# Optimization experiments

Measured on AMD Instinct MI355X. Metric: run time of the kernel, lower is better.

The kernel has to match this reference:

```python
import jax, jax.numpy as jnp
import numpy as np

B = 32768
H = 512
NH = 8
EPS = 1e-5


def _glorot(key, shape):
    fan_in, fan_out = shape[-1], shape[0]
    lim = (6.0 / (fan_in + fan_out)) ** 0.5
    return jax.random.uniform(key, shape, jnp.float32, -lim, lim)


def setup_inputs() -> dict:
    key = jax.random.key(0)
    ks = jax.random.split(key, 32)
    d = {
        "graph_features": jax.random.normal(ks[0], (B, H), jnp.float32),
        "seq_features": jax.random.normal(ks[1], (B, H), jnp.float32),
        "tabular_features": jax.random.normal(ks[2], (B, H), jnp.float32),
    }
    i = 3
    for name in ("g2s", "s2g", "t2m"):
        d[f"{name}_w_in"] = _glorot(ks[i], (3 * H, H)); i += 1
        d[f"{name}_b_in"] = jnp.zeros((3 * H,), jnp.float32)
        d[f"{name}_w_out"] = _glorot(ks[i], (H, H)); i += 1
        d[f"{name}_b_out"] = jnp.zeros((H,), jnp.float32)
    for name in ("gate_g", "gate_s", "gate_t"):
        d[f"{name}_w"] = _glorot(ks[i], (H, 2 * H)); i += 1
        d[f"{name}_b"] = jnp.zeros((H,), jnp.float32)
    d["fc1_w"] = _glorot(ks[i], (2 * H, 3 * H)); i += 1
    d["fc1_b"] = jnp.zeros((2 * H,), jnp.float32)
    d["ln_g"] = jnp.ones((2 * H,), jnp.float32)
    d["ln_b"] = jnp.zeros((2 * H,), jnp.float32)
    d["fc2_w"] = _glorot(ks[i], (H, 2 * H)); i += 1
    d["fc2_b"] = jnp.zeros((H,), jnp.float32)
    return d


def _mha(q, k, v, w_in, b_in, w_out, b_out):
    # q: [B,Sq,H], k/v: [B,Sk,H]. PyTorch nn.MultiheadAttention math (eval mode).
    dh = H // NH
    qp = q @ w_in[:H].T + b_in[:H]
    kp = k @ w_in[H:2 * H].T + b_in[H:2 * H]
    vp = v @ w_in[2 * H:].T + b_in[2 * H:]
    qh = qp.reshape(qp.shape[0], qp.shape[1], NH, dh)
    kh = kp.reshape(kp.shape[0], kp.shape[1], NH, dh)
    vh = vp.reshape(vp.shape[0], vp.shape[1], NH, dh)
    scores = jnp.einsum("bqhd,bkhd->bhqk", qh, kh) / jnp.sqrt(jnp.float32(dh))
    attn = jax.nn.softmax(scores, axis=-1)
    out = jnp.einsum("bhqk,bkhd->bqhd", attn, vh).reshape(q.shape[0], q.shape[1], H)
    return out @ w_out.T + b_out


def reference(graph_features, seq_features, tabular_features,
              g2s_w_in, g2s_b_in, g2s_w_out, g2s_b_out,
              s2g_w_in, s2g_b_in, s2g_w_out, s2g_b_out,
              t2m_w_in, t2m_b_in, t2m_w_out, t2m_b_out,
              gate_g_w, gate_g_b, gate_s_w, gate_s_b, gate_t_w, gate_t_b,
              fc1_w, fc1_b, ln_g, ln_b, fc2_w, fc2_b):
    g = graph_features[:, None, :]   # [B,1,H]
    s = seq_features[:, None, :]
    t = tabular_features[:, None, :]

    graph_to_seq = _mha(s, g, g, g2s_w_in, g2s_b_in, g2s_w_out, g2s_b_out)
    seq_to_graph = _mha(g, s, s, s2g_w_in, s2g_b_in, s2g_w_out, s2g_b_out)

    graph_gate = jax.nn.sigmoid(jnp.concatenate([g, seq_to_graph], -1) @ gate_g_w.T + gate_g_b)
    seq_gate = jax.nn.sigmoid(jnp.concatenate([s, graph_to_seq], -1) @ gate_s_w.T + gate_s_b)
    gated_graph = g * graph_gate
    gated_seq = s * seq_gate

    multimodal = jnp.concatenate([gated_graph, gated_seq], axis=1)  # [B,2,H]
    t2m = _mha(multimodal, t, t, t2m_w_in, t2m_b_in, t2m_w_out, t2m_b_out)  # [B,2,H]

    tab_comb = jnp.concatenate([t, t2m.mean(axis=1, keepdims=True)], -1)
    tab_gate = jax.nn.sigmoid(tab_comb @ gate_t_w.T + gate_t_b)
    gated_tab = t * tab_gate

    allf = jnp.concatenate([gated_graph[:, 0], gated_seq[:, 0], gated_tab[:, 0]], -1)  # [B,3H]
    h = allf @ fc1_w.T + fc1_b
    mu = h.mean(-1, keepdims=True)
    var = ((h - mu) ** 2).mean(-1, keepdims=True)
    h = (h - mu) / jnp.sqrt(var + EPS) * ln_g + ln_b
    h = jax.nn.relu(h)
    return h @ fc2_w.T + fc2_b
```

## Files before the change

### kernel.cpp

```cpp
#include <hip/hip_runtime.h>
#include <stdint.h>
#include <stddef.h>

#define MROWS 32768
#define HDIM  512
#define BM 128
#define BN 128
#define BK 64

typedef __attribute__((ext_vector_type(8))) _Float16 half8;
typedef __attribute__((ext_vector_type(4))) _Float16 half4v;
typedef __attribute__((ext_vector_type(4))) float    f32x4;

static __device__ __forceinline__ void gld_lds16(const void* g, void* l) {
    __builtin_amdgcn_global_load_lds(
        (__attribute__((address_space(1))) void*)(uintptr_t)g,
        (__attribute__((address_space(3))) void*)(uint32_t)(uintptr_t)l,
        16, 0, 0);
}

struct CvtJob  { const float* src; _Float16* dst; int srcld4, dstld, rowlen4, rows; };
struct CvtJobs { CvtJob j[11]; };

__global__ __launch_bounds__(256)
void cvt_rows(CvtJobs J) {
    const CvtJob jb = J.j[blockIdx.y];
    const int row = blockIdx.x;
    if (row >= jb.rows) return;
    const float4* __restrict__ s = (const float4*)jb.src + (size_t)row * jb.srcld4;
    _Float16* __restrict__ d = jb.dst + (size_t)row * jb.dstld;
    for (int c = threadIdx.x; c < jb.rowlen4; c += 256) {
        const float4 v = s[c];
        half4v o = { (_Float16)v.x, (_Float16)v.y, (_Float16)v.z, (_Float16)v.w };
        *(half4v*)(d + c * 4) = o;
    }
}

__global__ __launch_bounds__(384)
void cvt_chunk3(const float* __restrict__ x0, const float* __restrict__ x1,
                const float* __restrict__ x2, _Float16* __restrict__ dst) {
    const int row = blockIdx.x;
    const int mod = threadIdx.x >> 7;
    const int c   = threadIdx.x & 127;
    const float* s = (mod == 0) ? x0 : (mod == 1) ? x1 : x2;
    const float4 v = ((const float4*)(s + (size_t)row * 512))[c];
    half4v o = { (_Float16)v.x, (_Float16)v.y, (_Float16)v.z, (_Float16)v.w };
    *(half4v*)(dst + (size_t)row * 1536 + mod * 512 + c * 4) = o;
}

struct TcvtArgs { const float* src[3]; _Float16* dst; };
__global__ __launch_bounds__(256)
void tcvt512(TcvtArgs a) {
    __shared__ float t[32][33];
    const int m = blockIdx.z;
    const float* __restrict__ src = a.src[m];
    _Float16* __restrict__ dst = a.dst + (size_t)m * HDIM * HDIM;
    const int bx = blockIdx.x * 32, by = blockIdx.y * 32;
    const int tx = threadIdx.x & 31, ty = threadIdx.x >> 5;
    #pragma unroll
    for (int q = 0; q < 4; ++q)
        t[ty + q * 8][tx] = src[(size_t)(by + ty + q * 8) * 512 + bx + tx];
    __syncthreads();
    #pragma unroll
    for (int q = 0; q < 4; ++q)
        dst[(size_t)(bx + ty + q * 8) * 512 + by + tx] = (_Float16)t[tx][ty + q * 8];
}

struct MvArgs { const float* W[3]; const float* x[3]; const float* b[3]; float* y; int ldw, woff; };
__global__ __launch_bounds__(256)
void mv3(MvArgs a) {
    const int m = blockIdx.y;
    const int i = blockIdx.x * 256 + threadIdx.x;
    const float* __restrict__ W = a.W[m] + (size_t)i * a.ldw + a.woff;
    const float* __restrict__ x = a.x[m];
    float s = a.b[m][i];
    for (int j = 0; j < 512; ++j) s += W[j] * x[j];
    a.y[m * 512 + i] = s;
}

struct GemmP {
    const void* A1;
    const _Float16* W; const float* bias; void* C;
    int K, ldA1, ldw, ldc, coff;
    int zsA, zsW, zsC;
};

template<int EPI, int OCC>
__global__ __launch_bounds__(256, OCC)
void gemm_k(GemmP p) {
    __shared__ __align__(16) unsigned char smem[32768];
    _Float16* Asm = (_Float16*)smem;
    _Float16* Bsm = (_Float16*)(smem + 16384);

    const int tid  = threadIdx.x;
    const int wid  = tid >> 6;
    const int lane = tid & 63;
    const int m0 = blockIdx.x * BM;
    const int n0 = blockIdx.y * BN;
    const ptrdiff_t zz = blockIdx.z;
    const _Float16* __restrict__ A1h = (const _Float16*)((const char*)p.A1 + zz * p.zsA);
    const _Float16* __restrict__ Wp  = (const _Float16*)((const char*)p.W + zz * p.zsW);
    char* Cz = (char*)p.C + zz * p.zsC;

    const int wr = (wid >> 1) * 64;
    const int wc = (wid & 1) * 64;
    const int l15 = lane & 15;
    const int lhi = lane >> 4;

    f32x4 acc[4][4] = {};
    half8 xsave[8];
    const int colsel = (tid & 15) * 8;
    const int xtile  = n0 + (colsel & 64);
    const int xco    = colsel & 63;

    for (int kt = 0; kt < p.K; kt += BK) {
        #pragma unroll
        for (int i = 0; i < 4; ++i) {
            const int seg = wid * 256 + i * 64 + lane;
            const int row = seg >> 3;
            const int ke  = (seg & 7) * 8;
            gld_lds16(Wp  + (size_t)(n0 + row) * p.ldw  + kt + ke, &Bsm[seg * 8]);
            gld_lds16(A1h + (size_t)(m0 + row) * p.ldA1 + kt + ke, &Asm[seg * 8]);
        }
        __syncthreads();
        if (EPI == 1 && kt == xtile) {
            #pragma unroll
            for (int q = 0; q < 8; ++q)
                xsave[q] = *(const half8*)&Asm[(q * 16 + (tid >> 4)) * BK + xco];
        }
        #pragma unroll
        for (int kk = 0; kk < BK; kk += 32) {
            half8 fa[4], fb[4];
            #pragma unroll
            for (int i = 0; i < 4; ++i) {
                fa[i] = *(const half8*)&Asm[(wr + i * 16 + l15) * BK + kk + lhi * 8];
                fb[i] = *(const half8*)&Bsm[(wc + i * 16 + l15) * BK + kk + lhi * 8];
            }
            #pragma unroll
            for (int i = 0; i < 4; ++i)
                #pragma unroll
                for (int j = 0; j < 4; ++j)
                    acc[i][j] = __builtin_amdgcn_mfma_f32_16x16x32_f16(fa[i], fb[j], acc[i][j], 0, 0, 0);
        }
        __syncthreads();
    }

    if (EPI == 3) {
        float* Cf = (float*)smem;
        float* __restrict__ C = (float*)Cz;
        #pragma unroll
        for (int h = 0; h < 2; ++h) {
            if ((wr >> 6) == h) {
                #pragma unroll
                for (int j = 0; j < 4; ++j) {
                    const int col = wc + j * 16 + l15;
                    const float bia = p.bias ? p.bias[n0 + col] : 0.f;
                    #pragma unroll
                    for (int i = 0; i < 4; ++i)
                        #pragma unroll
                        for (int r = 0; r < 4; ++r)
                            Cf[(i * 16 + lhi * 4 + r) * 128 + col] = acc[i][j][r] + bia;
                }
            }
            __syncthreads();
            #pragma unroll
            for (int pph = 0; pph < 8; ++pph) {
                const int seg = pph * 256 + tid;
                const int row = seg >> 5, cs = seg & 31;
                const float4 v = *(const float4*)&Cf[row * 128 + cs * 4];
                *(float4*)&C[(size_t)(m0 + h * 64 + row) * p.ldc + n0 + cs * 4] = v;
            }
            __syncthreads();
        }
    } else {
        _Float16* Ct = (_Float16*)smem;
        #pragma unroll
        for (int j = 0; j < 4; ++j) {
            const int col = wc + j * 16 + l15;
            const float bia = (EPI == 2) ? 0.f : (p.bias ? p.bias[n0 + col] : 0.f);
            #pragma unroll
            for (int i = 0; i < 4; ++i)
                #pragma unroll
                for (int r = 0; r < 4; ++r) {
                    float v = acc[i][j][r] + bia;
                    if (EPI == 1) v = 1.f / (1.f + __expf(-v));
                    Ct[(wr + i * 16 + lhi * 4 + r) * 128 + col] = (_Float16)v;
                }
        }
        __syncthreads();
        _Float16* __restrict__ C = (_Float16*)Cz;
        #pragma unroll
        for (int pph = 0; pph < 8; ++pph) {
            const int seg = pph * 256 + tid;
            const int row = seg >> 4, cs = seg & 15;
            half8 hv = *(const half8*)&Ct[row * 128 + cs * 8];
            const size_t cidx = (size_t)(m0 + row) * p.ldc + p.coff + n0 + cs * 8;
            if (EPI == 1) hv = hv * xsave[pph];
            if (EPI == 2) { const half8 old = *(const half8*)&C[cidx]; hv = hv + old; }
            *(half8*)&C[cidx] = hv;
        }
    }
}

__global__ __launch_bounds__(256)
void ln_relu(_Float16* __restrict__ h, const float* __restrict__ gamma,
             const float* __restrict__ beta) {
    const int row  = blockIdx.x * 4 + (threadIdx.x >> 6);
    const int lane = threadIdx.x & 63;
    _Float16* hr = h + (size_t)row * 1024;
    const half8 v0 = *(const half8*)(hr + lane * 8);
    const half8 v1 = *(const half8*)(hr + 512 + lane * 8);
    float f0[8], f1[8];
    float s = 0.f, s2 = 0.f;
    #pragma unroll
    for (int j = 0; j < 8; ++j) {
        f0[j] = (float)v0[j]; s += f0[j]; s2 += f0[j] * f0[j];
        f1[j] = (float)v1[j]; s += f1[j]; s2 += f1[j] * f1[j];
    }
    #pragma unroll
    for (int off = 32; off > 0; off >>= 1) {
        s  += __shfl_xor(s,  off, 64);
        s2 += __shfl_xor(s2, off, 64);
    }
    const float mean = s * (1.f / 1024.f);
    const float var  = s2 * (1.f / 1024.f) - mean * mean;
    const float rstd = rsqrtf(var + 1e-5f);
    half8 o0, o1;
    #pragma unroll
    for (int j = 0; j < 8; ++j) {
        const int i0 = lane * 8 + j, i1 = 512 + lane * 8 + j;
        const float av = (f0[j] - mean) * rstd * gamma[i0] + beta[i0];
        const float bv = (f1[j] - mean) * rstd * gamma[i1] + beta[i1];
        o0[j] = (_Float16)(av > 0.f ? av : 0.f);
        o1[j] = (_Float16)(bv > 0.f ? bv : 0.f);
    }
    *(half8*)(hr + lane * 8) = o0;
    *(half8*)(hr + 512 + lane * 8) = o1;
}

__global__ __launch_bounds__(256)
void copy_f32(const float4* __restrict__ src, float4* __restrict__ dst, int n4) {
    const int stride = gridDim.x * blockDim.x;
    for (int i = blockIdx.x * blockDim.x + threadIdx.x; i < n4; i += stride)
        dst[i] = src[i];
}

extern "C" void kernel_launch(void* const* d_in, const int* in_sizes, int n_in,
                              void* d_out, int out_size, void* d_ws, size_t ws_size,
                              hipStream_t stream)
{
    (void)in_sizes; (void)n_in; (void)out_size;
    const size_t HH = (size_t)HDIM * HDIM;
    const size_t WBYTES = 25 * HH * 2 + 2 * 3 * 512 * 4;

    int CH = 16384;
    if (ws_size < 2 * (size_t)CH * 1536 * 2 + WBYTES) CH = 8192;
    if (ws_size < 2 * (size_t)CH * 1536 * 2 + WBYTES) return;
    const int nch = MROWS / CH;

    _Float16* wsH   = (_Float16*)d_ws;
    _Float16* slotB = wsH;
    _Float16* Xch   = slotB + (size_t)CH * 1536;
    _Float16* Wouth = Xch   + (size_t)CH * 1536;
    _Float16* Wg2h  = Wouth + 3 * HH;
    _Float16* WvT   = Wg2h  + 3 * HH;
    _Float16* WcoT  = WvT   + 3 * HH;
    _Float16* Wbig  = WcoT  + 3 * HH;
    _Float16* Wc2   = Wbig  + 4 * HH;
    _Float16* fc1h  = Wc2   + 1 * HH;
    _Float16* fc2h  = fc1h  + 6 * HH;
    float*    bco   = (float*)(fc2h + 2 * HH);
    float*    beff  = bco + 3 * 512;

    const float* X[3] = { (const float*)d_in[0], (const float*)d_in[1], (const float*)d_in[2] };
    const int asrc[3] = { 1, 0, 2 };

    CvtJobs cj;
    for (int m = 0; m < 3; ++m) {
        cj.j[m]     = { (const float*)d_in[5 + 4 * m], Wouth + m * HH, 128, 512, 128, 512 };
        cj.j[3 + m] = { (const float*)d_in[15 + 2 * m] + 512, Wg2h + m * HH, 256, 512, 128, 512 };
    }
    cj.j[6]  = { (const float*)d_in[15], Wbig,                    256, 1024, 128, 512 };
    cj.j[7]  = { (const float*)d_in[17], Wbig + 512 * 1024 + 512, 256, 1024, 128, 512 };
    cj.j[8]  = { (const float*)d_in[19], Wc2,                     256, 512,  128, 512 };
    cj.j[9]  = { (const float*)d_in[21], fc1h, 384, 1536, 384, 1024 };
    cj.j[10] = { (const float*)d_in[25], fc2h, 256, 1024, 256, 512 };
    cvt_rows<<<dim3(1024, 11, 1), 256, 0, stream>>>(cj);

    TcvtArgs ta;
    for (int m = 0; m < 3; ++m) ta.src[m] = (const float*)d_in[3 + 4 * m] + 2 * HH;
    ta.dst = WvT;
    tcvt512<<<dim3(16, 16, 3), 256, 0, stream>>>(ta);

    MvArgs mv;
    for (int m = 0; m < 3; ++m) {
        mv.W[m] = (const float*)d_in[5 + 4 * m];
        mv.x[m] = (const float*)d_in[4 + 4 * m] + 2 * HDIM;
        mv.b[m] = (const float*)d_in[6 + 4 * m];
    }
    mv.y = bco; mv.ldw = 512; mv.woff = 0;
    mv3<<<dim3(2, 3, 1), 256, 0, stream>>>(mv);

    GemmP p;
    p.bias = nullptr; p.coff = 0;
    p.zsA = p.zsW = p.zsC = 0;

    p.A1 = WvT; p.ldA1 = 512;
    p.W = Wouth; p.ldw = 512;
    p.C = WcoT; p.ldc = 512;
    p.K = 512;
    p.zsA = (int)(HH * 2); p.zsW = (int)(HH * 2); p.zsC = (int)(HH * 2);
    gemm_k<0, 4><<<dim3(4, 4, 3), 256, 0, stream>>>(p);

    p.A1 = Wg2h; p.zsA = (int)(HH * 2);
    p.W = WcoT + HH; p.zsW = -(int)(HH * 2);
    p.C = Wbig + 512; p.ldc = 1024; p.zsC = (int)((512 * 1024 - 512) * 2);
    gemm_k<0, 4><<<dim3(4, 4, 2), 256, 0, stream>>>(p);

    p.A1 = Wg2h + 2 * HH; p.zsA = 0;
    p.W = WcoT + 2 * HH; p.zsW = 0;
    p.C = Wc2; p.ldc = 512; p.zsC = 0;
    gemm_k<2, 4><<<dim3(4, 4, 1), 256, 0, stream>>>(p);

    for (int m = 0; m < 3; ++m) {
        mv.W[m] = (const float*)d_in[15 + 2 * m];
        mv.x[m] = bco + asrc[m] * 512;
        mv.b[m] = (const float*)d_in[16 + 2 * m];
    }
    mv.y = beff; mv.ldw = 1024; mv.woff = 512;
    mv3<<<dim3(2, 3, 1), 256, 0, stream>>>(mv);

    _Float16* hbuf = (_Float16*)d_out;
    for (int c = 0; c < nch; ++c) {
        const size_t roff = (size_t)c * CH;

        cvt_chunk3<<<dim3(CH, 1, 1), 384, 0, stream>>>(
            X[0] + roff * HDIM, X[1] + roff * HDIM, X[2] + roff * HDIM, Xch);

        p.A1 = Xch; p.ldA1 = 1536;
        p.W = Wbig; p.ldw = 1024;
        p.bias = beff;
        p.C = slotB; p.ldc = 1536; p.coff = 0;
        p.K = 1024;
        gemm_k<1, 3><<<dim3(CH / BM, 1024 / BN, 1), 256, 0, stream>>>(p);

        p.A1 = Xch + 1024; p.ldA1 = 1536;
        p.W = Wc2; p.ldw = 512;
        p.bias = beff + 1024;
        p.C = slotB; p.ldc = 1536; p.coff = 1024;
        p.K = 512;
        gemm_k<1, 3><<<dim3(CH / BM, HDIM / BN, 1), 256, 0, stream>>>(p);

        p.A1 = slotB; p.ldA1 = 1536;
        p.W = fc1h; p.ldw = 1536;
        p.bias = (const float*)d_in[22];
        p.C = hbuf + roff * 1024; p.ldc = 1024; p.coff = 0;
        p.K = 1536;
        gemm_k<0, 4><<<dim3(CH / BM, 1024 / BN, 1), 256, 0, stream>>>(p);
    }

    ln_relu<<<dim3(MROWS / 4, 1, 1), 256, 0, stream>>>(
        hbuf, (const float*)d_in[23], (const float*)d_in[24]);

    for (int c = 0; c < 2; ++c) {
        const size_t roff = (size_t)c * 16384;
        p.A1 = hbuf + roff * 1024; p.ldA1 = 1024;
        p.W = fc2h; p.ldw = 1024;
        p.bias = (const float*)d_in[26];
        p.C = d_ws; p.ldc = HDIM; p.coff = 0;
        p.K = 1024;
        gemm_k<3, 4><<<dim3(16384 / BM, HDIM / BN, 1), 256, 0, stream>>>(p);

        copy_f32<<<dim3(1024, 1, 1), 256, 0, stream>>>(
            (const float4*)d_ws, (float4*)d_out + roff * HDIM / 4,
            (int)((size_t)16384 * HDIM / 4));
    }
}
```

Baseline: 520.6 us.

## Merge gate GEMMs into one launch and write fc2 output directly

```diff
diff --git a/kernel.cpp b/kernel.cpp
--- a/kernel.cpp
+++ b/kernel.cpp
@@ -4,6 +4,7 @@
 
 #define MROWS 32768
 #define HDIM  512
+#define CH    16384
 #define BM 128
 #define BN 128
 #define BK 64
@@ -83,9 +84,11 @@
     const _Float16* W; const float* bias; void* C;
     int K, ldA1, ldw, ldc, coff;
     int zsA, zsW, zsC;
+    const void* A1b; const _Float16* Wb; const float* biasb;
+    int Kb, ldwb, coffb, nyb;
 };
 
-template<int EPI, int OCC>
+template<int EPI, int OCC, int MERGED>
 __global__ __launch_bounds__(256, OCC)
 void gemm_k(GemmP p) {
     __shared__ __align__(16) unsigned char smem[32768];
@@ -97,10 +100,24 @@
     const int lane = tid & 63;
     const int m0 = blockIdx.x * BM;
     const int n0 = blockIdx.y * BN;
-    const ptrdiff_t zz = blockIdx.z;
-    const _Float16* __restrict__ A1h = (const _Float16*)((const char*)p.A1 + zz * p.zsA);
-    const _Float16* __restrict__ Wp  = (const _Float16*)((const char*)p.W + zz * p.zsW);
-    char* Cz = (char*)p.C + zz * p.zsC;
+
+    const _Float16* __restrict__ A1h;
+    const _Float16* __restrict__ Wp;
+    const float* biasp;
+    char* Cz;
+    int K, ldA1, ldw, coff;
+    if (MERGED && blockIdx.z == 1) {
+        if ((int)blockIdx.y >= p.nyb) return;
+        A1h = (const _Float16*)p.A1b; Wp = p.Wb; biasp = p.biasb;
+        Cz = (char*)p.C; K = p.Kb; ldA1 = p.ldA1; ldw = p.ldwb; coff = p.coffb;
+    } else {
+        const ptrdiff_t zz = MERGED ? 0 : (ptrdiff_t)blockIdx.z;
+        A1h = (const _Float16*)((const char*)p.A1 + zz * p.zsA);
+        Wp  = (const _Float16*)((const char*)p.W + zz * p.zsW);
+        biasp = p.bias;
+        Cz = (char*)p.C + zz * p.zsC;
+        K = p.K; ldA1 = p.ldA1; ldw = p.ldw; coff = p.coff;
+    }
 
     const int wr = (wid >> 1) * 64;
     const int wc = (wid & 1) * 64;
@@ -113,14 +130,14 @@
     const int xtile  = n0 + (colsel & 64);
     const int xco    = colsel & 63;
 
-    for (int kt = 0; kt < p.K; kt += BK) {
+    for (int kt = 0; kt < K; kt += BK) {
         #pragma unroll
         for (int i = 0; i < 4; ++i) {
             const int seg = wid * 256 + i * 64 + lane;
             const int row = seg >> 3;
             const int ke  = (seg & 7) * 8;
-            gld_lds16(Wp  + (size_t)(n0 + row) * p.ldw  + kt + ke, &Bsm[seg * 8]);
-            gld_lds16(A1h + (size_t)(m0 + row) * p.ldA1 + kt + ke, &Asm[seg * 8]);
+            gld_lds16(Wp  + (size_t)(n0 + row) * ldw  + kt + ke, &Bsm[seg * 8]);
+            gld_lds16(A1h + (size_t)(m0 + row) * ldA1 + kt + ke, &Asm[seg * 8]);
         }
         __syncthreads();
         if (EPI == 1 && kt == xtile) {
@@ -154,7 +171,7 @@
                 #pragma unroll
                 for (int j = 0; j < 4; ++j) {
                     const int col = wc + j * 16 + l15;
-                    const float bia = p.bias ? p.bias[n0 + col] : 0.f;
+                    const float bia = biasp ? biasp[n0 + col] : 0.f;
                     #pragma unroll
                     for (int i = 0; i < 4; ++i)
                         #pragma unroll
@@ -177,7 +194,7 @@
         #pragma unroll
         for (int j = 0; j < 4; ++j) {
             const int col = wc + j * 16 + l15;
-            const float bia = (EPI == 2) ? 0.f : (p.bias ? p.bias[n0 + col] : 0.f);
+            const float bia = (EPI == 2) ? 0.f : (biasp ? biasp[n0 + col] : 0.f);
             #pragma unroll
             for (int i = 0; i < 4; ++i)
                 #pragma unroll
@@ -194,7 +211,7 @@
             const int seg = pph * 256 + tid;
             const int row = seg >> 4, cs = seg & 15;
             half8 hv = *(const half8*)&Ct[row * 128 + cs * 8];
-            const size_t cidx = (size_t)(m0 + row) * p.ldc + p.coff + n0 + cs * 8;
+            const size_t cidx = (size_t)(m0 + row) * p.ldc + coff + n0 + cs * 8;
             if (EPI == 1) hv = hv * xsave[pph];
             if (EPI == 2) { const half8 old = *(const half8*)&C[cidx]; hv = hv + old; }
             *(half8*)&C[cidx] = hv;
@@ -203,11 +220,12 @@
 }
 
 __global__ __launch_bounds__(256)
-void ln_relu(_Float16* __restrict__ h, const float* __restrict__ gamma,
-             const float* __restrict__ beta) {
+void ln_relu(const _Float16* __restrict__ hin, _Float16* __restrict__ hout,
+             const float* __restrict__ gamma, const float* __restrict__ beta) {
     const int row  = blockIdx.x * 4 + (threadIdx.x >> 6);
     const int lane = threadIdx.x & 63;
-    _Float16* hr = h + (size_t)row * 1024;
+    const _Float16* hr = hin + (size_t)row * 1024;
+    _Float16* ho = hout + (size_t)row * 1024;
     const half8 v0 = *(const half8*)(hr + lane * 8);
     const half8 v1 = *(const half8*)(hr + 512 + lane * 8);
     float f0[8], f1[8];
@@ -234,15 +252,8 @@
         o0[j] = (_Float16)(av > 0.f ? av : 0.f);
         o1[j] = (_Float16)(bv > 0.f ? bv : 0.f);
     }
-    *(half8*)(hr + lane * 8) = o0;
-    *(half8*)(hr + 512 + lane * 8) = o1;
-}
-
-__global__ __launch_bounds__(256)
-void copy_f32(const float4* __restrict__ src, float4* __restrict__ dst, int n4) {
-    const int stride = gridDim.x * blockDim.x;
-    for (int i = blockIdx.x * blockDim.x + threadIdx.x; i < n4; i += stride)
-        dst[i] = src[i];
+    *(half8*)(ho + lane * 8) = o0;
+    *(half8*)(ho + 512 + lane * 8) = o1;
 }
 
 extern "C" void kernel_launch(void* const* d_in, const int* in_sizes, int n_in,
@@ -251,12 +262,6 @@
 {
     (void)in_sizes; (void)n_in; (void)out_size;
     const size_t HH = (size_t)HDIM * HDIM;
-    const size_t WBYTES = 25 * HH * 2 + 2 * 3 * 512 * 4;
-
-    int CH = 16384;
-    if (ws_size < 2 * (size_t)CH * 1536 * 2 + WBYTES) CH = 8192;
-    if (ws_size < 2 * (size_t)CH * 1536 * 2 + WBYTES) return;
-    const int nch = MROWS / CH;
 
     _Float16* wsH   = (_Float16*)d_ws;
     _Float16* slotB = wsH;
@@ -271,6 +276,9 @@
     _Float16* fc2h  = fc1h  + 6 * HH;
     float*    bco   = (float*)(fc2h + 2 * HH);
     float*    beff  = bco + 3 * 512;
+    _Float16* hws   = wsH;
+    const size_t need = (size_t)((char*)(beff + 3 * 512) - (char*)d_ws);
+    if (ws_size < need) return;
 
     const float* X[3] = { (const float*)d_in[0], (const float*)d_in[1], (const float*)d_in[2] };
     const int asrc[3] = { 1, 0, 2 };
@@ -304,23 +312,25 @@
     GemmP p;
     p.bias = nullptr; p.coff = 0;
     p.zsA = p.zsW = p.zsC = 0;
+    p.A1b = nullptr; p.Wb = nullptr; p.biasb = nullptr;
+    p.Kb = 0; p.ldwb = 0; p.coffb = 0; p.nyb = 0;
 
     p.A1 = WvT; p.ldA1 = 512;
     p.W = Wouth; p.ldw = 512;
     p.C = WcoT; p.ldc = 512;
     p.K = 512;
     p.zsA = (int)(HH * 2); p.zsW = (int)(HH * 2); p.zsC = (int)(HH * 2);
-    gemm_k<0, 4><<<dim3(4, 4, 3), 256, 0, stream>>>(p);
+    gemm_k<0, 4, 0><<<dim3(4, 4, 3), 256, 0, stream>>>(p);
 
     p.A1 = Wg2h; p.zsA = (int)(HH * 2);
     p.W = WcoT + HH; p.zsW = -(int)(HH * 2);
     p.C = Wbig + 512; p.ldc = 1024; p.zsC = (int)((512 * 1024 - 512) * 2);
-    gemm_k<0, 4><<<dim3(4, 4, 2), 256, 0, stream>>>(p);
+    gemm_k<0, 4, 0><<<dim3(4, 4, 2), 256, 0, stream>>>(p);
 
     p.A1 = Wg2h + 2 * HH; p.zsA = 0;
     p.W = WcoT + 2 * HH; p.zsW = 0;
     p.C = Wc2; p.ldc = 512; p.zsC = 0;
-    gemm_k<2, 4><<<dim3(4, 4, 1), 256, 0, stream>>>(p);
+    gemm_k<2, 4, 0><<<dim3(4, 4, 1), 256, 0, stream>>>(p);
 
     for (int m = 0; m < 3; ++m) {
         mv.W[m] = (const float*)d_in[15 + 2 * m];
@@ -331,7 +341,7 @@
     mv3<<<dim3(2, 3, 1), 256, 0, stream>>>(mv);
 
     _Float16* hbuf = (_Float16*)d_out;
-    for (int c = 0; c < nch; ++c) {
+    for (int c = 0; c < 2; ++c) {
         const size_t roff = (size_t)c * CH;
 
         cvt_chunk3<<<dim3(CH, 1, 1), 384, 0, stream>>>(
@@ -342,37 +352,25 @@
         p.bias = beff;
         p.C = slotB; p.ldc = 1536; p.coff = 0;
         p.K = 1024;
-        gemm_k<1, 3><<<dim3(CH / BM, 1024 / BN, 1), 256, 0, stream>>>(p);
-
-        p.A1 = Xch + 1024; p.ldA1 = 1536;
-        p.W = Wc2; p.ldw = 512;
-        p.bias = beff + 1024;
-        p.C = slotB; p.ldc = 1536; p.coff = 1024;
-        p.K = 512;
-        gemm_k<1, 3><<<dim3(CH / BM, HDIM / BN, 1), 256, 0, stream>>>(p);
+        p.A1b = Xch + 1024; p.Wb = Wc2; p.biasb = beff + 1024;
+        p.Kb = 512; p.ldwb = 512; p.coffb = 1024; p.nyb = 4;
+        gemm_k<1, 3, 1><<<dim3(CH / BM, 1024 / BN, 2), 256, 0, stream>>>(p);
 
         p.A1 = slotB; p.ldA1 = 1536;
         p.W = fc1h; p.ldw = 1536;
         p.bias = (const float*)d_in[22];
         p.C = hbuf + roff * 1024; p.ldc = 1024; p.coff = 0;
         p.K = 1536;
-        gemm_k<0, 4><<<dim3(CH / BM, 1024 / BN, 1), 256, 0, stream>>>(p);
+        gemm_k<0, 4, 0><<<dim3(CH / BM, 1024 / BN, 1), 256, 0, stream>>>(p);
     }
 
     ln_relu<<<dim3(MROWS / 4, 1, 1), 256, 0, stream>>>(
-        hbuf, (const float*)d_in[23], (const float*)d_in[24]);
-
-    for (int c = 0; c < 2; ++c) {
-        const size_t roff = (size_t)c * 16384;
-        p.A1 = hbuf + roff * 1024; p.ldA1 = 1024;
-        p.W = fc2h; p.ldw = 1024;
-        p.bias = (const float*)d_in[26];
-        p.C = d_ws; p.ldc = HDIM; p.coff = 0;
-        p.K = 1024;
-        gemm_k<3, 4><<<dim3(16384 / BM, HDIM / BN, 1), 256, 0, stream>>>(p);
-
-        copy_f32<<<dim3(1024, 1, 1), 256, 0, stream>>>(
-            (const float4*)d_ws, (float4*)d_out + roff * HDIM / 4,
-            (int)((size_t)16384 * HDIM / 4));
-    }
-}
+        hbuf, hws, (const float*)d_in[23], (const float*)d_in[24]);
+
+    p.A1 = hws; p.ldA1 = 1024;
+    p.W = fc2h; p.ldw = 1024;
+    p.bias = (const float*)d_in[26];
+    p.C = d_out; p.ldc = HDIM; p.coff = 0;
+    p.K = 1024;
+    gemm_k<3, 4, 0><<<dim3(MROWS / BM, HDIM / BN, 1), 256, 0, stream>>>(p);
+}
```

Measured after the change: 454.1 us. 1.15x faster.

## Add 256x256 double-buffered swizzled GEMM and drop fc2 copy staging

Applied to the files above, without the earlier changes.

```diff
diff --git a/kernel.cpp b/kernel.cpp
--- a/kernel.cpp
+++ b/kernel.cpp
@@ -4,6 +4,7 @@
 
 #define MROWS 32768
 #define HDIM  512
+#define CH    16384
 #define BM 128
 #define BN 128
 #define BK 64
@@ -97,7 +98,7 @@
     const int lane = tid & 63;
     const int m0 = blockIdx.x * BM;
     const int n0 = blockIdx.y * BN;
-    const ptrdiff_t zz = blockIdx.z;
+    const ptrdiff_t zz = (ptrdiff_t)blockIdx.z;
     const _Float16* __restrict__ A1h = (const _Float16*)((const char*)p.A1 + zz * p.zsA);
     const _Float16* __restrict__ Wp  = (const _Float16*)((const char*)p.W + zz * p.zsW);
     char* Cz = (char*)p.C + zz * p.zsC;
@@ -108,10 +109,6 @@
     const int lhi = lane >> 4;
 
     f32x4 acc[4][4] = {};
-    half8 xsave[8];
-    const int colsel = (tid & 15) * 8;
-    const int xtile  = n0 + (colsel & 64);
-    const int xco    = colsel & 63;
 
     for (int kt = 0; kt < p.K; kt += BK) {
         #pragma unroll
@@ -123,11 +120,6 @@
             gld_lds16(A1h + (size_t)(m0 + row) * p.ldA1 + kt + ke, &Asm[seg * 8]);
         }
         __syncthreads();
-        if (EPI == 1 && kt == xtile) {
-            #pragma unroll
-            for (int q = 0; q < 8; ++q)
-                xsave[q] = *(const half8*)&Asm[(q * 16 + (tid >> 4)) * BK + xco];
-        }
         #pragma unroll
         for (int kk = 0; kk < BK; kk += 32) {
             half8 fa[4], fb[4];
@@ -195,19 +187,152 @@
             const int row = seg >> 4, cs = seg & 15;
             half8 hv = *(const half8*)&Ct[row * 128 + cs * 8];
             const size_t cidx = (size_t)(m0 + row) * p.ldc + p.coff + n0 + cs * 8;
-            if (EPI == 1) hv = hv * xsave[pph];
+            if (EPI == 1) {
+                const half8 xv = *(const half8*)(A1h + (size_t)(m0 + row) * p.ldA1
+                                                 + n0 + cs * 8);
+                hv = hv * xv;
+            }
             if (EPI == 2) { const half8 old = *(const half8*)&C[cidx]; hv = hv + old; }
             *(half8*)&C[cidx] = hv;
         }
     }
 }
 
+struct Gemm8P {
+    const _Float16* A; const _Float16* W; const float* bias; _Float16* C;
+    int K, ldA, ldW, ldc, coff;
+};
+
+template<int EPI>
+__global__ __launch_bounds__(512, 1)
+void gemm8(Gemm8P p) {
+    __shared__ __align__(16) unsigned char lds[131072];
+    char* LA = (char*)lds;
+    char* LB = (char*)lds + 65536;
+
+    const int tid  = threadIdx.x;
+    const int wid  = tid >> 6;
+    const int lane = tid & 63;
+    const int wm = wid >> 2;
+    const int wn = wid & 3;
+    const int l15 = lane & 15;
+    const int lhi = lane >> 4;
+    const int m0 = blockIdx.x * 256;
+    const int n0 = blockIdx.y * 256;
+    const _Float16* __restrict__ A = p.A;
+    const _Float16* __restrict__ W = p.W;
+    const int ldA = p.ldA, ldW = p.ldW;
+    const int nT = p.K >> 6;
+
+    f32x4 acc[8][4] = {};
+
+    auto stage = [&](int t) {
+        const int q = t & 1;
+        const int kt = t * 64;
+        #pragma unroll
+        for (int k = 0; k < 4; ++k) {
+            const int u = tid + k * 512;
+            const int row = u >> 3;
+            const int sc = (u & 7) ^ (row & 7);
+            gld_lds16(A + (size_t)(m0 + row) * ldA + kt + sc * 8,
+                      LA + ((size_t)q * 2048 + u) * 16);
+        }
+        #pragma unroll
+        for (int k = 0; k < 4; ++k) {
+            const int u = tid + k * 512;
+            const int row = u >> 3;
+            const int sc = (u & 7) ^ (row & 7);
+            gld_lds16(W + (size_t)(n0 + row) * ldW + kt + sc * 8,
+                      LB + ((size_t)q * 2048 + u) * 16);
+        }
+    };
+
+    stage(0);
+    asm volatile("s_waitcnt vmcnt(0)" ::: "memory");
+    __builtin_amdgcn_s_barrier();
+    asm volatile("" ::: "memory");
+
+    for (int t = 0; t < nT; ++t) {
+        const size_t aq = (size_t)(t & 1) * 2048 * 16;
+        half8 fb[4][2];
+        #pragma unroll
+        for (int ph = 0; ph < 4; ++ph) {
+            half8 fa[2][2];
+            if (ph == 0) {
+                #pragma unroll
+                for (int nf = 0; nf < 4; ++nf)
+                    #pragma unroll
+                    for (int kh = 0; kh < 2; ++kh) {
+                        const int row = wn * 64 + nf * 16 + l15;
+                        const int c16 = (kh * 4 + lhi) ^ (row & 7);
+                        fb[nf][kh] = *(const half8*)(LB + aq + ((size_t)row * 8 + c16) * 16);
+                    }
+            }
+            #pragma unroll
+            for (int mi = 0; mi < 2; ++mi)
+                #pragma unroll
+                for (int kh = 0; kh < 2; ++kh) {
+                    const int row = wm * 128 + (ph * 2 + mi) * 16 + l15;
+                    const int c16 = (kh * 4 + lhi) ^ (row & 7);
+                    fa[mi][kh] = *(const half8*)(LA + aq + ((size_t)row * 8 + c16) * 16);
+                }
+            if (ph == 0 && t + 1 < nT) stage(t + 1);
+            asm volatile("" ::: "memory");
+            __builtin_amdgcn_s_barrier();
+            asm volatile("s_waitcnt lgkmcnt(0)" ::: "memory");
+            __builtin_amdgcn_sched_barrier(0);
+            __builtin_amdgcn_s_setprio(1);
+            #pragma unroll
+            for (int mi = 0; mi < 2; ++mi)
+                #pragma unroll
+                for (int nf = 0; nf < 4; ++nf)
+                    #pragma unroll
+                    for (int kh = 0; kh < 2; ++kh)
+                        acc[ph * 2 + mi][nf] = __builtin_amdgcn_mfma_f32_16x16x32_f16(
+                            fa[mi][kh], fb[nf][kh], acc[ph * 2 + mi][nf], 0, 0, 0);
+            __builtin_amdgcn_s_setprio(0);
+            if (ph == 3) asm volatile("s_waitcnt vmcnt(0)" ::: "memory");
+            asm volatile("" ::: "memory");
+            __builtin_amdgcn_s_barrier();
+            asm volatile("" ::: "memory");
+        }
+    }
+
+    _Float16* Ct = (_Float16*)lds;
+    #pragma unroll
+    for (int mf = 0; mf < 8; ++mf)
+        #pragma unroll
+        for (int nf = 0; nf < 4; ++nf) {
+            const int col = wn * 64 + nf * 16 + l15;
+            const float bia = p.bias[n0 + col];
+            #pragma unroll
+            for (int r = 0; r < 4; ++r) {
+                float v = acc[mf][nf][r] + bia;
+                if (EPI == 1) v = 1.f / (1.f + __expf(-v));
+                Ct[(wm * 128 + mf * 16 + lhi * 4 + r) * 256 + col] = (_Float16)v;
+            }
+        }
+    __syncthreads();
+    #pragma unroll
+    for (int it = 0; it < 16; ++it) {
+        const int u = it * 512 + tid;
+        const int row = u >> 5, cs = u & 31;
+        half8 hv = *(const half8*)&Ct[row * 256 + cs * 8];
+        if (EPI == 1) {
+            const half8 xv = *(const half8*)(A + (size_t)(m0 + row) * ldA + n0 + cs * 8);
+            hv = hv * xv;
+        }
+        *(half8*)&p.C[(size_t)(m0 + row) * p.ldc + p.coff + n0 + cs * 8] = hv;
+    }
+}
+
 __global__ __launch_bounds__(256)
-void ln_relu(_Float16* __restrict__ h, const float* __restrict__ gamma,
-             const float* __restrict__ beta) {
+void ln_relu(const _Float16* __restrict__ hin, _Float16* __restrict__ hout,
+             const float* __restrict__ gamma, const float* __restrict__ beta) {
     const int row  = blockIdx.x * 4 + (threadIdx.x >> 6);
     const int lane = threadIdx.x & 63;
-    _Float16* hr = h + (size_t)row * 1024;
+    const _Float16* hr = hin + (size_t)row * 1024;
+    _Float16* ho = hout + (size_t)row * 1024;
     const half8 v0 = *(const half8*)(hr + lane * 8);
     const half8 v1 = *(const half8*)(hr + 512 + lane * 8);
     float f0[8], f1[8];
@@ -234,15 +359,8 @@
         o0[j] = (_Float16)(av > 0.f ? av : 0.f);
         o1[j] = (_Float16)(bv > 0.f ? bv : 0.f);
     }
-    *(half8*)(hr + lane * 8) = o0;
-    *(half8*)(hr + 512 + lane * 8) = o1;
-}
-
-__global__ __launch_bounds__(256)
-void copy_f32(const float4* __restrict__ src, float4* __restrict__ dst, int n4) {
-    const int stride = gridDim.x * blockDim.x;
-    for (int i = blockIdx.x * blockDim.x + threadIdx.x; i < n4; i += stride)
-        dst[i] = src[i];
+    *(half8*)(ho + lane * 8) = o0;
+    *(half8*)(ho + 512 + lane * 8) = o1;
 }
 
 extern "C" void kernel_launch(void* const* d_in, const int* in_sizes, int n_in,
@@ -251,12 +369,6 @@
 {
     (void)in_sizes; (void)n_in; (void)out_size;
     const size_t HH = (size_t)HDIM * HDIM;
-    const size_t WBYTES = 25 * HH * 2 + 2 * 3 * 512 * 4;
-
-    int CH = 16384;
-    if (ws_size < 2 * (size_t)CH * 1536 * 2 + WBYTES) CH = 8192;
-    if (ws_size < 2 * (size_t)CH * 1536 * 2 + WBYTES) return;
-    const int nch = MROWS / CH;
 
     _Float16* wsH   = (_Float16*)d_ws;
     _Float16* slotB = wsH;
@@ -271,6 +383,9 @@
     _Float16* fc2h  = fc1h  + 6 * HH;
     float*    bco   = (float*)(fc2h + 2 * HH);
     float*    beff  = bco + 3 * 512;
+    _Float16* hws   = wsH;
+    const size_t need = (size_t)((char*)(beff + 3 * 512) - (char*)d_ws);
+    if (ws_size < need) return;
 
     const float* X[3] = { (const float*)d_in[0], (const float*)d_in[1], (const float*)d_in[2] };
     const int asrc[3] = { 1, 0, 2 };
@@ -331,48 +446,42 @@
     mv3<<<dim3(2, 3, 1), 256, 0, stream>>>(mv);
 
     _Float16* hbuf = (_Float16*)d_out;
-    for (int c = 0; c < nch; ++c) {
+    Gemm8P g8;
+    for (int c = 0; c < 2; ++c) {
         const size_t roff = (size_t)c * CH;
 
         cvt_chunk3<<<dim3(CH, 1, 1), 384, 0, stream>>>(
             X[0] + roff * HDIM, X[1] + roff * HDIM, X[2] + roff * HDIM, Xch);
 
-        p.A1 = Xch; p.ldA1 = 1536;
-        p.W = Wbig; p.ldw = 1024;
-        p.bias = beff;
-        p.C = slotB; p.ldc = 1536; p.coff = 0;
-        p.K = 1024;
-        gemm_k<1, 3><<<dim3(CH / BM, 1024 / BN, 1), 256, 0, stream>>>(p);
+        g8.A = Xch; g8.ldA = 1536;
+        g8.W = Wbig; g8.ldW = 1024;
+        g8.bias = beff;
+        g8.C = slotB; g8.ldc = 1536; g8.coff = 0;
+        g8.K = 1024;
+        gemm8<1><<<dim3(CH / 256, 4, 1), 512, 0, stream>>>(g8);
 
         p.A1 = Xch + 1024; p.ldA1 = 1536;
         p.W = Wc2; p.ldw = 512;
         p.bias = beff + 1024;
         p.C = slotB; p.ldc = 1536; p.coff = 1024;
-        p.K = 512;
-        gemm_k<1, 3><<<dim3(CH / BM, HDIM / BN, 1), 256, 0, stream>>>(p);
-
-        p.A1 = slotB; p.ldA1 = 1536;
-        p.W = fc1h; p.ldw = 1536;
-        p.bias = (const float*)d_in[22];
-        p.C = hbuf + roff * 1024; p.ldc = 1024; p.coff = 0;
-        p.K = 1536;
-        gemm_k<0, 4><<<dim3(CH / BM, 1024 / BN, 1), 256, 0, stream>>>(p);
+        p.K = 512; p.zsA = p.zsW = p.zsC = 0;
+        gemm_k<1, 4><<<dim3(CH / BM, 4, 1), 256, 0, stream>>>(p);
+
+        g8.A = slotB; g8.ldA = 1536;
+        g8.W = fc1h; g8.ldW = 1536;
+        g8.bias = (const float*)d_in[22];
+        g8.C = hbuf + roff * 1024; g8.ldc = 1024; g8.coff = 0;
+        g8.K = 1536;
+        gemm8<0><<<dim3(CH / 256, 4, 1), 512, 0, stream>>>(g8);
     }
 
     ln_relu<<<dim3(MROWS / 4, 1, 1), 256, 0, stream>>>(
-        hbuf, (const float*)d_in[23], (const float*)d_in[24]);
-
-    for (int c = 0; c < 2; ++c) {
-        const size_t roff = (size_t)c * 16384;
-        p.A1 = hbuf + roff * 1024; p.ldA1 = 1024;
-        p.W = fc2h; p.ldw = 1024;
-        p.bias = (const float*)d_in[26];
-        p.C = d_ws; p.ldc = HDIM; p.coff = 0;
-        p.K = 1024;
-        gemm_k<3, 4><<<dim3(16384 / BM, HDIM / BN, 1), 256, 0, stream>>>(p);
-
-        copy_f32<<<dim3(1024, 1, 1), 256, 0, stream>>>(
-            (const float4*)d_ws, (float4*)d_out + roff * HDIM / 4,
-            (int)((size_t)16384 * HDIM / 4));
-    }
-}
+        hbuf, hws, (const float*)d_in[23], (const float*)d_in[24]);
+
+    p.A1 = hws; p.ldA1 = 1024;
+    p.W = fc2h; p.ldw = 1024;
+    p.bias = (const float*)d_in[26];
+    p.C = d_out; p.ldc = HDIM; p.coff = 0;
+    p.K = 1024; p.zsA = p.zsW = p.zsC = 0;
+    gemm_k<3, 4><<<dim3(MROWS / BM, HDIM / BN, 1), 256, 0, stream>>>(p);
+}
```

After: 457.1 us, median of 2. 12.2% less time.
